# Optimization experiments

Hardware: AMD Instinct MI355X
Metric: run time of the kernel (lower is better)

Reference implementation:

```python
import jax, jax.numpy as jnp
import numpy as np

TEMPERATURE = 0.07


def sparsemax(z):
    """Sparsemax along the last axis (Martins & Astudillo, 2016)."""
    n = z.shape[-1]
    z_sorted = -jnp.sort(-z, axis=-1)                      # descending sort
    k = jnp.arange(1, n + 1, dtype=z.dtype)
    cum = jnp.cumsum(z_sorted, axis=-1)
    support = (1.0 + k * z_sorted) > cum                   # support set indicator
    k_z = jnp.sum(support, axis=-1, keepdims=True)         # support size per row
    idx = k_z.astype(jnp.int32) - 1
    cum_kz = jnp.take_along_axis(cum, idx, axis=-1)
    tau = (cum_kz - 1.0) / k_z.astype(z.dtype)             # threshold
    return jnp.maximum(z - tau, 0.0)


def setup_inputs() -> dict:
    key = jax.random.key(0)
    k1, k2 = jax.random.split(key)
    B, V, D = 2048, 2, 128
    features = jax.random.normal(k1, (B, V, D), dtype=jnp.float32)
    attention_scores = jax.random.normal(k2, (V * B, V * B), dtype=jnp.float32)
    return {"features": features, "attention_scores": attention_scores}


def reference(features, attention_scores):
    B, V, D = features.shape
    N = V * B
    dt = features.dtype

    # default mask path (labels=None, mask=None): identity over the batch
    mask = jnp.eye(B, dtype=dt)

    # L2-normalize features along feature dim, flatten views (row-major, as torch .view)
    f = features / jnp.linalg.norm(features, axis=-1, keepdims=True)
    f = f.reshape(N, D)

    # cosine similarities / temperature, row-max subtracted (detached)
    sim = jnp.matmul(f, f.T) / TEMPERATURE                  # [N, N]
    sim = sim - jax.lax.stop_gradient(jnp.max(sim, axis=-1, keepdims=True))

    big_mask = jnp.tile(mask, (V, V))                       # mask.repeat(V, V)
    eye_n = jnp.eye(N, dtype=dt)
    positive_mask = big_mask - eye_n
    negative_mask = 1.0 - big_mask

    masked_scores = sparsemax((attention_scores * negative_mask) / TEMPERATURE)

    exp_sim = jnp.exp(sim) * (positive_mask + negative_mask - masked_scores)
    log_prob = sim - jnp.log(jnp.sum(exp_sim, axis=-1, keepdims=True))

    mean_log_prob_pos = jnp.sum(log_prob * positive_mask, axis=1) / jnp.sum(positive_mask, axis=1)
    loss = -jnp.mean(mean_log_prob_pos)                     # reduction='mean'
    return loss, masked_scores
```

## Files before the change

kernel.cpp:

```cpp
#include <hip/hip_runtime.h>
#include <math.h>

#define NN   4096
#define BD   2048
#define DF   128
#define INV_T (1.0f/0.07f)
#define CAND_CAP 128

typedef __attribute__((ext_vector_type(8))) short short8v;
typedef __attribute__((ext_vector_type(4))) float float4v;
typedef float f4a __attribute__((ext_vector_type(4), aligned(4)));

__device__ inline unsigned short f2bf_rne(float x) {
  unsigned int u = __float_as_uint(x);
  u = (u + 0x7FFFu + ((u >> 16) & 1u)) >> 16;
  return (unsigned short)u;
}

__global__ __launch_bounds__(256) void k_sparsemax(
    const float* __restrict__ attn,
    const float* __restrict__ feat,
    unsigned short* __restrict__ fbf,
    float* __restrict__ msOut,
    float* __restrict__ Zv) {
  __shared__ float redM[4];
  __shared__ float cand[CAND_CAP];
  __shared__ int   cidx[CAND_CAP];
  __shared__ int ccnt;
  __shared__ float tauS;
  __shared__ float corrS[4];
  __shared__ float2 fN[64];
  int row  = blockIdx.x;
  int tid  = threadIdx.x;
  int lane = tid & 63, wv = tid >> 6;

  if (wv == 0) {
    float2 v = ((const float2*)(feat + (size_t)row * DF))[lane];
    float ss = v.x * v.x + v.y * v.y;
    #pragma unroll
    for (int off = 1; off < 64; off <<= 1) ss += __shfl_xor(ss, off, 64);
    float inv = rsqrtf(ss);
    float2 nv; nv.x = v.x * inv; nv.y = v.y * inv;
    ushort2 o; o.x = f2bf_rne(nv.x); o.y = f2bf_rne(nv.y);
    ((ushort2*)(fbf + (size_t)row * DF))[lane] = o;
    fN[lane] = nv;
  }

  const float4* arow = (const float4*)(attn + (size_t)row * NN);
  int rb = row & (BD - 1);
  float z[16];
  #pragma unroll
  for (int u = 0; u < 4; ++u) {
    int q = u * 256 + tid;
    float4 a = arow[q];
    int j = q * 4;
    z[4*u+0] = (((j+0) & (BD-1)) == rb) ? 0.f : a.x * INV_T;
    z[4*u+1] = (((j+1) & (BD-1)) == rb) ? 0.f : a.y * INV_T;
    z[4*u+2] = (((j+2) & (BD-1)) == rb) ? 0.f : a.z * INV_T;
    z[4*u+3] = (((j+3) & (BD-1)) == rb) ? 0.f : a.w * INV_T;
  }
  float m = z[0];
  #pragma unroll
  for (int u = 1; u < 16; ++u) m = fmaxf(m, z[u]);
  #pragma unroll
  for (int off = 1; off < 64; off <<= 1) m = fmaxf(m, __shfl_xor(m, off, 64));
  if (lane == 0) redM[wv] = m;
  if (tid == 0) ccnt = 0;
  __syncthreads();
  m = fmaxf(fmaxf(redM[0], redM[1]), fmaxf(redM[2], redM[3]));

  float thresh = m - 1.0f;
  #pragma unroll
  for (int u = 0; u < 4; ++u) {
    #pragma unroll
    for (int t = 0; t < 4; ++t) {
      if (z[4*u+t] > thresh) {
        int slot = atomicAdd(&ccnt, 1);
        if (slot < CAND_CAP) {
          cand[slot] = z[4*u+t];
          cidx[slot] = (u * 256 + tid) * 4 + t;
        }
      }
    }
  }
  __syncthreads();

  if (tid == 0) {
    int nc = min(ccnt, CAND_CAP);
    float tau = thresh;
    #pragma unroll 1
    for (int it = 0; it < 32; ++it) {
      float S = 0.f; float C = 0.f;
      for (int e = 0; e < nc; ++e) {
        float v = cand[e];
        if (v > tau) { S += v; C += 1.f; }
      }
      float nt = (C > 0.f) ? (S - 1.0f) / C : tau;
      if (nt == tau) break;
      tau = nt;
    }
    tauS = tau;
  }
  __syncthreads();
  float tau = tauS;

  float* orow = msOut + (size_t)row * NN;
  #pragma unroll
  for (int u = 0; u < 4; ++u) {
    int j = (u * 256 + tid) * 4;
    f4a v;
    v.x = fmaxf(z[4*u+0] - tau, 0.f);
    v.y = fmaxf(z[4*u+1] - tau, 0.f);
    v.z = fmaxf(z[4*u+2] - tau, 0.f);
    v.w = fmaxf(z[4*u+3] - tau, 0.f);
    *((f4a*)(orow + j)) = v;
  }

  int nc = min(ccnt, CAND_CAP);
  float2 fi = fN[lane];
  float corr = 0.f;
  for (int e = wv; e < nc; e += 4) {
    float msv = cand[e] - tau;
    if (msv <= 0.f) continue;
    int j = cidx[e];
    float2 g = ((const float2*)(feat + (size_t)j * DF))[lane];
    float dt = fi.x * g.x + fi.y * g.y;
    float sj = g.x * g.x + g.y * g.y;
    #pragma unroll
    for (int off = 1; off < 64; off <<= 1) {
      dt += __shfl_xor(dt, off, 64);
      sj += __shfl_xor(sj, off, 64);
    }
    float s = dt * rsqrtf(sj);
    corr += __expf(s * INV_T - INV_T) * msv;
  }
  if (lane == 0) corrS[wv] = corr;
  __syncthreads();
  if (tid == 0) {
    float tot = (corrS[0] + corrS[1]) + (corrS[2] + corrS[3]);
    Zv[row] = -tot;
  }
}

__global__ __launch_bounds__(256) void k_gram(
    const unsigned short* __restrict__ fbf, float* __restrict__ Zv,
    float* __restrict__ numer) {
  int t = blockIdx.x, bi = 0, L = 32;
  while (t >= L) { t -= L; --L; ++bi; }
  int bj = bi + t;

  int tid = threadIdx.x;
  int wave = tid >> 6, lane = tid & 63;
  int c = lane & 15, quad = lane >> 4;
  int wi = wave >> 1, wj = wave & 1;
  if (bi == bj && wi > wj) return;
  int i0 = bi * 128 + wi * 64;
  int j0 = bj * 128 + wj * 64;

  const unsigned short* aBase = fbf + (size_t)(i0 + c) * DF + quad * 8;
  const unsigned short* bBase = fbf + (size_t)(j0 + c) * DF + quad * 8;

  float4v acc[4][4];
  #pragma unroll
  for (int m = 0; m < 4; ++m)
    #pragma unroll
    for (int n = 0; n < 4; ++n) acc[m][n] = (float4v){0.f, 0.f, 0.f, 0.f};

  #pragma unroll
  for (int k0 = 0; k0 < DF; k0 += 32) {
    short8v afr[4], bfr[4];
    #pragma unroll
    for (int m = 0; m < 4; ++m)
      afr[m] = *(const short8v*)(aBase + (size_t)(m * 16) * DF + k0);
    #pragma unroll
    for (int n = 0; n < 4; ++n)
      bfr[n] = *(const short8v*)(bBase + (size_t)(n * 16) * DF + k0);
    #pragma unroll
    for (int m = 0; m < 4; ++m)
      #pragma unroll
      for (int n = 0; n < 4; ++n)
        acc[m][n] = __builtin_amdgcn_mfma_f32_16x16x32_bf16(
            afr[m], bfr[n], acc[m][n], 0, 0, 0);
  }

  float colacc[4] = {0.f, 0.f, 0.f, 0.f};
  #pragma unroll
  for (int m = 0; m < 4; ++m) {
    #pragma unroll
    for (int r = 0; r < 4; ++r) {
      int i = i0 + m * 16 + quad * 4 + r;
      float zrow = 0.f;
      #pragma unroll
      for (int n = 0; n < 4; ++n) {
        int j = j0 + n * 16 + c;
        float simv = acc[m][n][r] * INV_T - INV_T;
        float e = (j > i) ? __expf(simv) : 0.f;
        zrow += e;
        colacc[n] += e;
        if (j - i == BD) { numer[i] = simv; numer[j] = simv; }
      }
      zrow += __shfl_xor(zrow, 1, 64);
      zrow += __shfl_xor(zrow, 2, 64);
      zrow += __shfl_xor(zrow, 4, 64);
      zrow += __shfl_xor(zrow, 8, 64);
      if (c == 0) atomicAdd(&Zv[i], zrow);
    }
  }
  #pragma unroll
  for (int n = 0; n < 4; ++n) {
    float v = colacc[n];
    v += __shfl_xor(v, 16, 64);
    v += __shfl_xor(v, 32, 64);
    if (quad == 0) atomicAdd(&Zv[j0 + n * 16 + c], v);
  }
}

__global__ void k_loss(const float* __restrict__ Zv,
                       const float* __restrict__ numer,
                       float* __restrict__ out) {
  float acc = 0.f;
  for (int i = threadIdx.x; i < NN; i += 256)
    acc += numer[i] - logf(Zv[i]);
  #pragma unroll
  for (int off = 1; off < 64; off <<= 1) acc += __shfl_xor(acc, off, 64);
  __shared__ float red[4];
  int wv = threadIdx.x >> 6, lane = threadIdx.x & 63;
  if (lane == 0) red[wv] = acc;
  __syncthreads();
  if (threadIdx.x == 0) {
    float t = (red[0] + red[1]) + (red[2] + red[3]);
    out[0] = -t / (float)NN;
  }
}

extern "C" void kernel_launch(void* const* d_in, const int* in_sizes, int n_in,
                              void* d_out, int out_size, void* d_ws, size_t ws_size,
                              hipStream_t stream) {
  const float* feat = (const float*)d_in[0];
  const float* attn = (const float*)d_in[1];
  float* out = (float*)d_out;
  float* msOut = out + 1;

  float* Zv    = (float*)d_ws;
  float* numer = Zv + NN;
  unsigned short* fbf = (unsigned short*)(numer + NN);

  k_sparsemax<<<dim3(4096), dim3(256), 0, stream>>>(attn, feat, fbf, msOut, Zv);
  k_gram<<<dim3(528), dim3(256), 0, stream>>>(fbf, Zv, numer);
  k_loss<<<dim3(1), dim3(256), 0, stream>>>(Zv, numer, out);
}
```

Baseline: 147.9 us.

## Fuse loss reduction into gram kernel via last-block counter; nontemporal attn I/O

Removes the separate single-block loss kernel. The gram kernel now finishes with a global completion counter: whichever block finishes last does the final log-sum reduction. The counter is reset by the sparsemax kernel. The sparsemax kernel also switches its attention-score loads and masked-score stores to nontemporal builtins, to avoid polluting caches on the 64MB streamed in and out. This saves one launch and the gap between kernels, at the cost of an atomic and fences in every gram block.

```diff
diff --git a/kernel.cpp b/kernel.cpp
--- a/kernel.cpp
+++ b/kernel.cpp
@@ -6,10 +6,12 @@
 #define DF   128
 #define INV_T (1.0f/0.07f)
 #define CAND_CAP 128
+#define GRAM_BLOCKS 528
 
 typedef __attribute__((ext_vector_type(8))) short short8v;
 typedef __attribute__((ext_vector_type(4))) float float4v;
 typedef float f4a __attribute__((ext_vector_type(4), aligned(4)));
+typedef float f4n __attribute__((ext_vector_type(4)));
 
 __device__ inline unsigned short f2bf_rne(float x) {
   unsigned int u = __float_as_uint(x);
@@ -22,7 +24,8 @@
     const float* __restrict__ feat,
     unsigned short* __restrict__ fbf,
     float* __restrict__ msOut,
-    float* __restrict__ Zv) {
+    float* __restrict__ Zv,
+    unsigned int* __restrict__ doneCnt) {
   __shared__ float redM[4];
   __shared__ float cand[CAND_CAP];
   __shared__ int   cidx[CAND_CAP];
@@ -34,6 +37,8 @@
   int tid  = threadIdx.x;
   int lane = tid & 63, wv = tid >> 6;
 
+  if (row == 0 && tid == 0) *doneCnt = 0u;
+
   if (wv == 0) {
     float2 v = ((const float2*)(feat + (size_t)row * DF))[lane];
     float ss = v.x * v.x + v.y * v.y;
@@ -46,13 +51,13 @@
     fN[lane] = nv;
   }
 
-  const float4* arow = (const float4*)(attn + (size_t)row * NN);
+  const f4n* arow = (const f4n*)(attn + (size_t)row * NN);
   int rb = row & (BD - 1);
   float z[16];
   #pragma unroll
   for (int u = 0; u < 4; ++u) {
     int q = u * 256 + tid;
-    float4 a = arow[q];
+    f4n a = __builtin_nontemporal_load(arow + q);
     int j = q * 4;
     z[4*u+0] = (((j+0) & (BD-1)) == rb) ? 0.f : a.x * INV_T;
     z[4*u+1] = (((j+1) & (BD-1)) == rb) ? 0.f : a.y * INV_T;
@@ -113,7 +118,7 @@
     v.y = fmaxf(z[4*u+1] - tau, 0.f);
     v.z = fmaxf(z[4*u+2] - tau, 0.f);
     v.w = fmaxf(z[4*u+3] - tau, 0.f);
-    *((f4a*)(orow + j)) = v;
+    __builtin_nontemporal_store(v, (f4a*)(orow + j));
   }
 
   int nc = min(ccnt, CAND_CAP);
@@ -144,7 +149,8 @@
 
 __global__ __launch_bounds__(256) void k_gram(
     const unsigned short* __restrict__ fbf, float* __restrict__ Zv,
-    float* __restrict__ numer) {
+    float* __restrict__ numer, unsigned int* __restrict__ doneCnt,
+    float* __restrict__ out) {
   int t = blockIdx.x, bi = 0, L = 32;
   while (t >= L) { t -= L; --L; ++bi; }
   int bj = bi + t;
@@ -153,83 +159,100 @@
   int wave = tid >> 6, lane = tid & 63;
   int c = lane & 15, quad = lane >> 4;
   int wi = wave >> 1, wj = wave & 1;
-  if (bi == bj && wi > wj) return;
-  int i0 = bi * 128 + wi * 64;
-  int j0 = bj * 128 + wj * 64;
-
-  const unsigned short* aBase = fbf + (size_t)(i0 + c) * DF + quad * 8;
-  const unsigned short* bBase = fbf + (size_t)(j0 + c) * DF + quad * 8;
-
-  float4v acc[4][4];
-  #pragma unroll
-  for (int m = 0; m < 4; ++m)
-    #pragma unroll
-    for (int n = 0; n < 4; ++n) acc[m][n] = (float4v){0.f, 0.f, 0.f, 0.f};
-
-  #pragma unroll
-  for (int k0 = 0; k0 < DF; k0 += 32) {
-    short8v afr[4], bfr[4];
+  bool dead = (bi == bj && wi > wj);
+  if (!dead) {
+    int i0 = bi * 128 + wi * 64;
+    int j0 = bj * 128 + wj * 64;
+
+    const unsigned short* aBase = fbf + (size_t)(i0 + c) * DF + quad * 8;
+    const unsigned short* bBase = fbf + (size_t)(j0 + c) * DF + quad * 8;
+
+    float4v acc[4][4];
     #pragma unroll
     for (int m = 0; m < 4; ++m)
-      afr[m] = *(const short8v*)(aBase + (size_t)(m * 16) * DF + k0);
-    #pragma unroll
-    for (int n = 0; n < 4; ++n)
-      bfr[n] = *(const short8v*)(bBase + (size_t)(n * 16) * DF + k0);
-    #pragma unroll
-    for (int m = 0; m < 4; ++m)
+      #pragma unroll
+      for (int n = 0; n < 4; ++n) acc[m][n] = (float4v){0.f, 0.f, 0.f, 0.f};
+
+    #pragma unroll
+    for (int k0 = 0; k0 < DF; k0 += 32) {
+      short8v afr[4], bfr[4];
+      #pragma unroll
+      for (int m = 0; m < 4; ++m)
+        afr[m] = *(const short8v*)(aBase + (size_t)(m * 16) * DF + k0);
       #pragma unroll
       for (int n = 0; n < 4; ++n)
-        acc[m][n] = __builtin_amdgcn_mfma_f32_16x16x32_bf16(
-            afr[m], bfr[n], acc[m][n], 0, 0, 0);
-  }
-
-  float colacc[4] = {0.f, 0.f, 0.f, 0.f};
-  #pragma unroll
-  for (int m = 0; m < 4; ++m) {
-    #pragma unroll
-    for (int r = 0; r < 4; ++r) {
-      int i = i0 + m * 16 + quad * 4 + r;
-      float zrow = 0.f;
-      #pragma unroll
-      for (int n = 0; n < 4; ++n) {
-        int j = j0 + n * 16 + c;
-        float simv = acc[m][n][r] * INV_T - INV_T;
-        float e = (j > i) ? __expf(simv) : 0.f;
-        zrow += e;
-        colacc[n] += e;
-        if (j - i == BD) { numer[i] = simv; numer[j] = simv; }
+        bfr[n] = *(const short8v*)(bBase + (size_t)(n * 16) * DF + k0);
+      #pragma unroll
+      for (int m = 0; m < 4; ++m)
+        #pragma unroll
+        for (int n = 0; n < 4; ++n)
+          acc[m][n] = __builtin_amdgcn_mfma_f32_16x16x32_bf16(
+              afr[m], bfr[n], acc[m][n], 0, 0, 0);
+    }
+
+    float colacc[4] = {0.f, 0.f, 0.f, 0.f};
+    #pragma unroll
+    for (int m = 0; m < 4; ++m) {
+      #pragma unroll
+      for (int r = 0; r < 4; ++r) {
+        int i = i0 + m * 16 + quad * 4 + r;
+        float zrow = 0.f;
+        #pragma unroll
+        for (int n = 0; n < 4; ++n) {
+          int j = j0 + n * 16 + c;
+          float simv = acc[m][n][r] * INV_T - INV_T;
+          float e = (j > i) ? __expf(simv) : 0.f;
+          zrow += e;
+          colacc[n] += e;
+          if (j - i == BD) {
+            __hip_atomic_store(&numer[i], simv, __ATOMIC_RELAXED,
+                               __HIP_MEMORY_SCOPE_AGENT);
+            __hip_atomic_store(&numer[j], simv, __ATOMIC_RELAXED,
+                               __HIP_MEMORY_SCOPE_AGENT);
+          }
+        }
+        zrow += __shfl_xor(zrow, 1, 64);
+        zrow += __shfl_xor(zrow, 2, 64);
+        zrow += __shfl_xor(zrow, 4, 64);
+        zrow += __shfl_xor(zrow, 8, 64);
+        if (c == 0) atomicAdd(&Zv[i], zrow);
       }
-      zrow += __shfl_xor(zrow, 1, 64);
-      zrow += __shfl_xor(zrow, 2, 64);
-      zrow += __shfl_xor(zrow, 4, 64);
-      zrow += __shfl_xor(zrow, 8, 64);
-      if (c == 0) atomicAdd(&Zv[i], zrow);
-    }
-  }
-  #pragma unroll
-  for (int n = 0; n < 4; ++n) {
-    float v = colacc[n];
-    v += __shfl_xor(v, 16, 64);
-    v += __shfl_xor(v, 32, 64);
-    if (quad == 0) atomicAdd(&Zv[j0 + n * 16 + c], v);
-  }
-}
-
-__global__ void k_loss(const float* __restrict__ Zv,
-                       const float* __restrict__ numer,
-                       float* __restrict__ out) {
-  float acc = 0.f;
-  for (int i = threadIdx.x; i < NN; i += 256)
-    acc += numer[i] - logf(Zv[i]);
-  #pragma unroll
-  for (int off = 1; off < 64; off <<= 1) acc += __shfl_xor(acc, off, 64);
+    }
+    #pragma unroll
+    for (int n = 0; n < 4; ++n) {
+      float v = colacc[n];
+      v += __shfl_xor(v, 16, 64);
+      v += __shfl_xor(v, 32, 64);
+      if (quad == 0) atomicAdd(&Zv[j0 + n * 16 + c], v);
+    }
+  }
+
+  __shared__ unsigned int isLast;
   __shared__ float red[4];
-  int wv = threadIdx.x >> 6, lane = threadIdx.x & 63;
-  if (lane == 0) red[wv] = acc;
-  __syncthreads();
-  if (threadIdx.x == 0) {
-    float t = (red[0] + red[1]) + (red[2] + red[3]);
-    out[0] = -t / (float)NN;
+  if (tid == 0) {
+    __threadfence();
+    unsigned int old = atomicAdd(doneCnt, 1u);
+    isLast = (old == GRAM_BLOCKS - 1) ? 1u : 0u;
+  }
+  __syncthreads();
+  if (isLast) {
+    __threadfence();
+    float acc = 0.f;
+    for (int i = tid; i < NN; i += 256) {
+      float nu = __hip_atomic_load(&numer[i], __ATOMIC_RELAXED,
+                                   __HIP_MEMORY_SCOPE_AGENT);
+      float zz = __hip_atomic_load(&Zv[i], __ATOMIC_RELAXED,
+                                   __HIP_MEMORY_SCOPE_AGENT);
+      acc += nu - logf(zz);
+    }
+    #pragma unroll
+    for (int off = 1; off < 64; off <<= 1) acc += __shfl_xor(acc, off, 64);
+    if (lane == 0) red[wave] = acc;
+    __syncthreads();
+    if (tid == 0) {
+      float tt = (red[0] + red[1]) + (red[2] + red[3]);
+      out[0] = -tt / (float)NN;
+    }
   }
 }
 
@@ -243,9 +266,11 @@
 
   float* Zv    = (float*)d_ws;
   float* numer = Zv + NN;
-  unsigned short* fbf = (unsigned short*)(numer + NN);
-
-  k_sparsemax<<<dim3(4096), dim3(256), 0, stream>>>(attn, feat, fbf, msOut, Zv);
-  k_gram<<<dim3(528), dim3(256), 0, stream>>>(fbf, Zv, numer);
-  k_loss<<<dim3(1), dim3(256), 0, stream>>>(Zv, numer, out);
-}
+  unsigned int* doneCnt = (unsigned int*)(numer + NN);
+  unsigned short* fbf = (unsigned short*)(doneCnt + 64);
+
+  k_sparsemax<<<dim3(4096), dim3(256), 0, stream>>>(attn, feat, fbf, msOut, Zv,
+                                                    doneCnt);
+  k_gram<<<dim3(GRAM_BLOCKS), dim3(256), 0, stream>>>(fbf, Zv, numer, doneCnt,
+                                                      out);
+}
```

Result: slower. 158.6 us (+7.2%).
